# Kernel tuning notes

Measured on AMD Instinct MI355X. Metric: run time of the kernel, lower is better.

Reference implementation:

```python
import jax, jax.numpy as jnp
import numpy as np

NEG_SLOPE = 0.2  # PyG GATConv default negative_slope


def _gat_conv(x, edge_index, W, a_src, a_dst, b, concat):
    """One PyG-style GATConv layer (eval mode, add_self_loops=True).
    x: [N, F_in], W: [F_in, H*C], a_src/a_dst: [H, C], b: [H*C] or [C].
    """
    N = x.shape[0]
    H, C = a_src.shape
    loops = jnp.arange(N, dtype=edge_index.dtype)
    src = jnp.concatenate([edge_index[0], loops])  # [E+N]
    dst = jnp.concatenate([edge_index[1], loops])
    h = (x @ W).reshape(N, H, C)                   # [N,H,C]
    al_s = jnp.einsum('nhc,hc->nh', h, a_src)      # [N,H]
    al_d = jnp.einsum('nhc,hc->nh', h, a_dst)
    e = jax.nn.leaky_relu(al_s[src] + al_d[dst], NEG_SLOPE)  # [E+N, H]
    # segment softmax over incoming edges of each dst node
    m = jax.lax.stop_gradient(jax.ops.segment_max(e, dst, num_segments=N))
    ex = jnp.exp(e - m[dst])
    denom = jax.ops.segment_sum(ex, dst, num_segments=N)
    alpha = ex / denom[dst]                        # [E+N, H]
    out = jax.ops.segment_sum(h[src] * alpha[:, :, None], dst, num_segments=N)  # [N,H,C]
    out = out.reshape(N, H * C) if concat else out.mean(axis=1)
    return out + b


def setup_inputs() -> dict:
    key = jax.random.key(0)
    ks = jax.random.split(key, 10)
    N, E, F_IN = 100000, 1600000, 128
    H1, C1 = 4, 32   # layer 1: concat -> 128
    H2, C2 = 1, 64   # layer 2: mean   -> 64
    x = jax.random.normal(ks[0], (N, F_IN), dtype=jnp.float32)
    edge_index = jax.random.randint(ks[1], (2, E), 0, N, dtype=jnp.int32)
    s = 0.1
    return {
        'x': x,
        'edge_index': edge_index,
        'W1': jax.random.normal(ks[2], (F_IN, H1 * C1), dtype=jnp.float32) * s,
        'a1_src': jax.random.normal(ks[3], (H1, C1), dtype=jnp.float32) * s,
        'a1_dst': jax.random.normal(ks[4], (H1, C1), dtype=jnp.float32) * s,
        'b1': jnp.zeros((H1 * C1,), dtype=jnp.float32),
        'W2': jax.random.normal(ks[5], (H1 * C1, H2 * C2), dtype=jnp.float32) * s,
        'a2_src': jax.random.normal(ks[6], (H2, C2), dtype=jnp.float32) * s,
        'a2_dst': jax.random.normal(ks[7], (H2, C2), dtype=jnp.float32) * s,
        'b2': jnp.zeros((C2,), dtype=jnp.float32),
    }


def reference(x, edge_index, W1, a1_src, a1_dst, b1, W2, a2_src, a2_dst, b2):
    h = _gat_conv(x, edge_index, W1, a1_src, a1_dst, b1, concat=True)   # [N,128]
    h = jax.nn.elu(h)                                                   # dropout is identity in eval
    out = _gat_conv(h, edge_index, W2, a2_src, a2_dst, b2, concat=False)  # [N,64]
    return out
```

## Files before the change

kernel.cpp:

```cpp
#include <hip/hip_runtime.h>
#include <hip/hip_bf16.h>
#include <math.h>

static constexpr float NEG_SLOPE = 0.2f;
static constexpr float NEG_BIG = -3.0e38f;

typedef __attribute__((ext_vector_type(8))) short short8;
typedef __attribute__((ext_vector_type(4))) float f32x4;

__device__ __forceinline__ float blo(unsigned u) { return __uint_as_float(u << 16); }
__device__ __forceinline__ float bhi(unsigned u) { return __uint_as_float(u & 0xffff0000u); }
__device__ __forceinline__ float bhiraw(unsigned u) { return __uint_as_float(u); }
__device__ __forceinline__ unsigned pack2(float a, float b) {
  __hip_bfloat162 t = __float22bfloat162_rn(make_float2(a, b));
  union { __hip_bfloat162 b; unsigned u; } v;
  v.b = t;
  return v.u;
}

#define FMA8(V, A)                         \
  acc[0] = fmaf(blo((V).x), (A), acc[0]);  \
  acc[1] = fmaf(bhi((V).x), (A), acc[1]);  \
  acc[2] = fmaf(blo((V).y), (A), acc[2]);  \
  acc[3] = fmaf(bhi((V).y), (A), acc[3]);  \
  acc[4] = fmaf(blo((V).z), (A), acc[4]);  \
  acc[5] = fmaf(bhi((V).z), (A), acc[5]);  \
  acc[6] = fmaf(blo((V).w), (A), acc[6]);  \
  acc[7] = fmaf(bhi((V).w), (A), acc[7])

#define FMA8R(V, A)                           \
  acc[0] = fmaf(blo((V).x), (A), acc[0]);     \
  acc[1] = fmaf(bhiraw((V).x), (A), acc[1]);  \
  acc[2] = fmaf(blo((V).y), (A), acc[2]);     \
  acc[3] = fmaf(bhiraw((V).y), (A), acc[3]);  \
  acc[4] = fmaf(blo((V).z), (A), acc[4]);     \
  acc[5] = fmaf(bhiraw((V).z), (A), acc[5]);  \
  acc[6] = fmaf(blo((V).w), (A), acc[6]);     \
  acc[7] = fmaf(bhiraw((V).w), (A), acc[7])

template <int BN, int HEADS>
__device__ void prep_w(const float* __restrict__ W, const float* __restrict__ as_,
                       const float* __restrict__ ad_, uint4* __restrict__ out, int i) {
  constexpr int XC = BN + 16;
  constexpr int C = BN / HEADS;
  if (i >= XC * 16) return;
  const int col = i >> 4;
  const int chunk = (i & 15) ^ (col & 7);
  float v[8];
  if (col < BN) {
#pragma unroll
    for (int t = 0; t < 8; ++t) v[t] = W[(size_t)(chunk * 8 + t) * BN + col];
  } else {
    const int j = col - BN;
#pragma unroll
    for (int t = 0; t < 8; ++t) v[t] = 0.f;
    if (j < 2 * HEADS) {
      const int hh = (HEADS == 4) ? (j & 3) : 0;
      const bool is_src = (HEADS == 4) ? (j < 4) : (j == 0);
      const float* av = (is_src ? as_ : ad_) + hh * C;
      const float* wb = W + hh * C;
#pragma unroll
      for (int t = 0; t < 8; ++t) {
        float s = 0.f;
        for (int c = 0; c < C; ++c) s = fmaf(wb[(size_t)(chunk * 8 + t) * BN + c], av[c], s);
        v[t] = s;
      }
    }
  }
  uint4 u;
  u.x = pack2(v[0], v[1]);
  u.y = pack2(v[2], v[3]);
  u.z = pack2(v[4], v[5]);
  u.w = pack2(v[6], v[7]);
  out[i] = u;
}

__global__ void k_setup(const float* __restrict__ W1, const float* __restrict__ a1s,
                        const float* __restrict__ a1d, uint4* __restrict__ wsw1,
                        const float* __restrict__ W2, const float* __restrict__ a2s,
                        const float* __restrict__ a2d, uint4* __restrict__ wsw2,
                        int* __restrict__ cnt, int N) {
  const int b = blockIdx.x;
  const int tid = threadIdx.x;
  if (b < 9) {
    prep_w<128, 4>(W1, a1s, a1d, wsw1, b * 256 + tid);
  } else if (b < 14) {
    prep_w<64, 1>(W2, a2s, a2d, wsw2, (b - 9) * 256 + tid);
  } else {
    const int i = (b - 14) * 256 + tid;
    if (i < (N >> 2)) ((int4*)cnt)[i] = make_int4(0, 0, 0, 0);
    const int r = (N & ~3) + i;
    if (i < 4 && r < N) cnt[r] = 0;
  }
}

template <int BN, int HEADS>
__global__ __launch_bounds__(256) void k_mfma_gemm(
    const float* __restrict__ x, const uint4* __restrict__ wsw,
    __hip_bfloat16* __restrict__ h_out, float* __restrict__ als,
    float* __restrict__ ald, int N) {
  constexpr int XC = BN + 16;
  constexpr int NTILES = BN / 16;
  constexpr int BUFSZ = (XC * 256 > 128 * 256) ? XC * 256 : 128 * 256;
  __shared__ unsigned char buf[BUFSZ];
  const int tid = threadIdx.x;
  const int lane = tid & 63;
  const int wid = tid >> 6;
  const int base = blockIdx.x * 128;

  for (int it = 0; it < 8; ++it) {
    const int i = it * 256 + tid;
    const int r = i >> 4, c = i & 15;
    const int g = base + r;
    float4 f0 = make_float4(0.f, 0.f, 0.f, 0.f), f1 = f0;
    if (g < N) {
      const float* xp = x + (size_t)g * 128 + c * 8;
      f0 = *(const float4*)xp;
      f1 = *(const float4*)(xp + 4);
    }
    uint4 u;
    u.x = pack2(f0.x, f0.y);
    u.y = pack2(f0.z, f0.w);
    u.z = pack2(f1.x, f1.y);
    u.w = pack2(f1.z, f1.w);
    *(uint4*)(buf + r * 256 + ((c * 16) ^ ((r & 7) << 4))) = u;
  }
  __syncthreads();

  const int lg = lane >> 4;
  const int ll = lane & 15;
  union U { uint4 u; short8 s; };
  short8 afr[2][4];
#pragma unroll
  for (int rt = 0; rt < 2; ++rt) {
    const int row = wid * 32 + rt * 16 + ll;
    const unsigned char* rp = buf + row * 256;
    const int swz = (row & 7) << 4;
#pragma unroll
    for (int ks = 0; ks < 4; ++ks) {
      U t;
      t.u = *(const uint4*)(rp + ((ks * 64 + lg * 16) ^ swz));
      afr[rt][ks] = t.s;
    }
  }
  __syncthreads();

  {
    uint4* dst = (uint4*)buf;
    for (int i = tid; i < XC * 16; i += 256) dst[i] = wsw[i];
  }
  __syncthreads();

  f32x4 acc[2][NTILES + 1];
#pragma unroll
  for (int rt = 0; rt < 2; ++rt)
#pragma unroll
    for (int t = 0; t <= NTILES; ++t) acc[rt][t] = (f32x4){0.f, 0.f, 0.f, 0.f};

#pragma unroll
  for (int t = 0; t <= NTILES; ++t) {
    const int col = t * 16 + ll;
    const unsigned char* cp = buf + col * 256;
    const int swz = (col & 7) << 4;
#pragma unroll
    for (int ks = 0; ks < 4; ++ks) {
      U b;
      b.u = *(const uint4*)(cp + ((ks * 64 + lg * 16) ^ swz));
      acc[0][t] = __builtin_amdgcn_mfma_f32_16x16x32_bf16(afr[0][ks], b.s, acc[0][t], 0, 0, 0);
      acc[1][t] = __builtin_amdgcn_mfma_f32_16x16x32_bf16(afr[1][ks], b.s, acc[1][t], 0, 0, 0);
    }
  }

#pragma unroll
  for (int rt = 0; rt < 2; ++rt) {
#pragma unroll
    for (int r = 0; r < 4; ++r) {
      const int row = base + wid * 32 + rt * 16 + lg * 4 + r;
      if (row < N) {
        const float v = acc[rt][NTILES][r];
        if (HEADS == 4) {
          if (ll < 4) als[(size_t)row * 4 + ll] = v;
          else if (ll < 8) ald[(size_t)row * 4 + (ll - 4)] = v;
        } else {
          if (ll == 0) als[row] = v;
          else if (ll == 1) ald[row] = v;
        }
      }
    }
  }

  __syncthreads();
#pragma unroll
  for (int rt = 0; rt < 2; ++rt) {
#pragma unroll
    for (int t = 0; t < NTILES; ++t) {
#pragma unroll
      for (int r = 0; r < 4; ++r) {
        const float v = acc[rt][t][r];
        const float vn = __shfl_xor(v, 1, 64);
        if (!(lane & 1)) {
          const int row = wid * 32 + rt * 16 + lg * 4 + r;
          *(unsigned*)(buf + row * (BN * 2) + (t * 16 + ll) * 2) = pack2(v, vn);
        }
      }
    }
  }
  __syncthreads();
  {
    constexpr int U4 = 128 * BN / 8;
    constexpr int U4R = BN / 8;
    for (int i = tid; i < U4; i += 256) {
      const int row = i / U4R;
      const int g = base + row;
      if (g < N)
        *(uint4*)((unsigned short*)h_out + (size_t)g * BN + (i % U4R) * 8) = ((uint4*)buf)[i];
    }
  }
}

__global__ void k_count(const int* __restrict__ edst, int* __restrict__ cnt, int E) {
  int i = blockIdx.x * blockDim.x + threadIdx.x;
  if (i < E) atomicAdd(cnt + edst[i], 1);
}

__global__ void k_scan_local(const int* __restrict__ cnt, int* __restrict__ rowptr,
                             int* __restrict__ bsum, int N) {
  __shared__ int lds[256];
  const int tid = threadIdx.x;
  const int base = blockIdx.x * 1024;
  int vals[4], tsum = 0;
#pragma unroll
  for (int q = 0; q < 4; ++q) {
    int i = base + tid * 4 + q;
    vals[q] = (i < N) ? cnt[i] + 1 : 0;
    tsum += vals[q];
  }
  lds[tid] = tsum;
  __syncthreads();
  for (int off = 1; off < 256; off <<= 1) {
    int t = (tid >= off) ? lds[tid - off] : 0;
    __syncthreads();
    lds[tid] += t;
    __syncthreads();
  }
  int run = lds[tid] - tsum;
  if (tid == 255) bsum[blockIdx.x] = lds[255];
#pragma unroll
  for (int q = 0; q < 4; ++q) {
    int i = base + tid * 4 + q;
    if (i < N) rowptr[i] = run;
    run += vals[q];
  }
}

__global__ void k_scan_add2(const int* __restrict__ bsum, int nb,
                            int* __restrict__ rowptr, int* __restrict__ cursor,
                            int N, int total) {
  __shared__ int pref[128];
  const int tid = threadIdx.x;
  int own = 0;
  if (tid < 128) {
    own = (tid < nb) ? bsum[tid] : 0;
    pref[tid] = own;
  }
  __syncthreads();
  for (int off = 1; off < 128; off <<= 1) {
    int t = (tid >= off && tid < 128) ? pref[tid - off] : 0;
    __syncthreads();
    if (tid < 128) pref[tid] += t;
    __syncthreads();
  }
  if (tid < 128) pref[tid] -= own;
  __syncthreads();
  const int i = blockIdx.x * blockDim.x + tid;
  if (i < N) {
    int r = rowptr[i] + pref[i >> 10];
    rowptr[i] = r;
    cursor[i] = r;
  } else if (i == N) {
    rowptr[N] = total;
  }
}

__global__ void k_build_part(const int* __restrict__ esrc, const int* __restrict__ edst,
                             int* __restrict__ cursor, int* __restrict__ nbr, int E, int N) {
  constexpr int NPARTS = 4;
  const int p = blockIdx.x & 3;
  const int span = (N + NPARTS - 1) / NPARTS;
  const int lo = p * span;
  const int hi = min(N, lo + span);
  const int gid = (int)(blockIdx.x >> 2) * blockDim.x + threadIdx.x;
  const int stride = (int)(gridDim.x >> 2) * blockDim.x;
  const int E4 = E >> 2;
  for (int i = gid; i < E4; i += stride) {
    const int4 d4 = ((const int4*)edst)[i];
    const int4 s4 = ((const int4*)esrc)[i];
    if (d4.x >= lo && d4.x < hi) nbr[atomicAdd(cursor + d4.x, 1)] = s4.x;
    if (d4.y >= lo && d4.y < hi) nbr[atomicAdd(cursor + d4.y, 1)] = s4.y;
    if (d4.z >= lo && d4.z < hi) nbr[atomicAdd(cursor + d4.z, 1)] = s4.z;
    if (d4.w >= lo && d4.w < hi) nbr[atomicAdd(cursor + d4.w, 1)] = s4.w;
  }
  for (int i = E4 * 4 + gid; i < E + N; i += stride) {
    const int d = i < E ? edst[i] : i - E;
    if (d >= lo && d < hi) {
      const int sn = i < E ? esrc[i] : i - E;
      nbr[atomicAdd(cursor + d, 1)] = sn;
    }
  }
}

__global__ void k_gather_l1(const int* __restrict__ rowptr, const int* __restrict__ nbr,
                            const float* __restrict__ als, const float* __restrict__ ald,
                            const __hip_bfloat16* __restrict__ hfeat,
                            const float* __restrict__ bias,
                            float* __restrict__ out, int N) {
  __shared__ float atab[4][2][4][40];
  __shared__ unsigned otab[4][2][32];
  const int lane = threadIdx.x & 63;
  const int wid = threadIdx.x >> 6;
  const int half = lane >> 5;
  const int l32 = lane & 31;
  const int node = (int)((blockIdx.x * blockDim.x + threadIdx.x) >> 6) * 2 + half;
  const bool valid = node < N;
  int start = 0, end = 0;
  if (valid) {
    start = rowptr[node];
    end = rowptr[node + 1];
  }
  const int deg = end - start;
  const float4 aldd = valid ? ((const float4*)ald)[node] : make_float4(0.f, 0.f, 0.f, 0.f);

  float t[4];
  int myn = 0;
  {
    const int j = start + l32;
    if (j < end) {
      myn = nbr[j];
      const float4 av = ((const float4*)als)[myn];
      const float tr[4] = {av.x + aldd.x, av.y + aldd.y, av.z + aldd.z, av.w + aldd.w};
#pragma unroll
      for (int h = 0; h < 4; ++h) t[h] = tr[h] >= 0.f ? tr[h] : NEG_SLOPE * tr[h];
    } else {
#pragma unroll
      for (int h = 0; h < 4; ++h) t[h] = NEG_BIG;
    }
  }
  otab[wid][half][l32] = (unsigned)myn << 8;

  float Mh[4], rden[4], myex[4];
  if (deg <= 32) {
#pragma unroll
    for (int h = 0; h < 4; ++h) {
      float M = t[h];
#pragma unroll
      for (int off = 1; off < 32; off <<= 1) M = fmaxf(M, __shfl_xor(M, off, 64));
      const float e = __expf(t[h] - M);
      float sum = e;
#pragma unroll
      for (int off = 1; off < 32; off <<= 1) sum += __shfl_xor(sum, off, 64);
      Mh[h] = M;
      rden[h] = 1.f / sum;
      myex[h] = e * rden[h];
    }
  } else {
    float m[4], s[4];
#pragma unroll
    for (int h = 0; h < 4; ++h) {
      m[h] = t[h];
      s[h] = (t[h] > NEG_BIG) ? 1.f : 0.f;
    }
    for (int b = start + 32; b < end; b += 32) {
      const int j = b + l32;
      if (j < end) {
        const int sn = nbr[j];
        const float4 av = ((const float4*)als)[sn];
        const float tr[4] = {av.x + aldd.x, av.y + aldd.y, av.z + aldd.z, av.w + aldd.w};
#pragma unroll
        for (int h = 0; h < 4; ++h) {
          const float tv = tr[h] >= 0.f ? tr[h] : NEG_SLOPE * tr[h];
          const float M = fmaxf(m[h], tv);
          s[h] = s[h] * __expf(m[h] - M) + __expf(tv - M);
          m[h] = M;
        }
      }
    }
#pragma unroll
    for (int h = 0; h < 4; ++h) {
      float M = m[h];
#pragma unroll
      for (int off = 1; off < 32; off <<= 1) M = fmaxf(M, __shfl_xor(M, off, 64));
      float e = s[h] * __expf(m[h] - M);
#pragma unroll
      for (int off = 1; off < 32; off <<= 1) e += __shfl_xor(e, off, 64);
      Mh[h] = M;
      rden[h] = 1.f / e;
      myex[h] = __expf(t[h] - M) * rden[h];
    }
  }
#pragma unroll
  for (int h = 0; h < 4; ++h) atab[wid][half][h][l32] = myex[h];

  const int sub = l32 >> 4;
  const int q = l32 & 15;
  const int head = q >> 2;
  const char* hq = (const char*)hfeat + q * 16;
  float acc[8];
#pragma unroll
  for (int k = 0; k < 8; ++k) acc[k] = 0.f;

  const int nq = deg < 32 ? deg : 32;
  const float* ap = &atab[wid][half][head][0];
  const unsigned* op = &otab[wid][half][0];
  for (int j0 = 0; j0 < nq; j0 += 8) {
    const float a0 = ap[j0 + sub];
    const float a1 = ap[j0 + 2 + sub];
    const float a2 = ap[j0 + 4 + sub];
    const float a3 = ap[j0 + 6 + sub];
    const uint4 v0 = *(const uint4*)(hq + op[j0 + sub]);
    const uint4 v1 = *(const uint4*)(hq + op[j0 + 2 + sub]);
    const uint4 v2 = *(const uint4*)(hq + op[j0 + 4 + sub]);
    const uint4 v3 = *(const uint4*)(hq + op[j0 + 6 + sub]);
    FMA8R(v0, a0);
    FMA8R(v1, a1);
    FMA8R(v2, a2);
    FMA8R(v3, a3);
  }
  if (deg > 32) {
    const float Mm = head == 0 ? Mh[0] : head == 1 ? Mh[1] : head == 2 ? Mh[2] : Mh[3];
    const float rd = head == 0 ? rden[0] : head == 1 ? rden[1] : head == 2 ? rden[2] : rden[3];
    const float ad_ = head == 0 ? aldd.x : head == 1 ? aldd.y : head == 2 ? aldd.z : aldd.w;
    for (int j0 = 32; j0 < deg; j0 += 2) {
      const int j = j0 + sub;
      float a = 0.f;
      int sn = 0;
      if (j < deg) {
        sn = nbr[start + j];
        const float4 av = ((const float4*)als)[sn];
        const float as_ = head == 0 ? av.x : head == 1 ? av.y : head == 2 ? av.z : av.w;
        float tv = as_ + ad_;
        tv = tv >= 0.f ? tv : NEG_SLOPE * tv;
        a = __expf(tv - Mm) * rd;
      }
      const uint4 v = *(const uint4*)(hq + (size_t)sn * 256);
      FMA8R(v, a);
    }
  }

#pragma unroll
  for (int k = 0; k < 8; ++k) acc[k] += __shfl_xor(acc[k], 16, 64);
  if (valid && sub == 0) {
    const float4 b0 = ((const float4*)bias)[q * 2];
    const float4 b1 = ((const float4*)bias)[q * 2 + 1];
    float r[8] = {acc[0] + b0.x, acc[1] + b0.y, acc[2] + b0.z, acc[3] + b0.w,
                  acc[4] + b1.x, acc[5] + b1.y, acc[6] + b1.z, acc[7] + b1.w};
#pragma unroll
    for (int k = 0; k < 8; ++k) r[k] = r[k] > 0.f ? r[k] : __expf(r[k]) - 1.f;
    float4* opo = (float4*)(out + (size_t)node * 128 + q * 8);
    opo[0] = make_float4(r[0], r[1], r[2], r[3]);
    opo[1] = make_float4(r[4], r[5], r[6], r[7]);
  }
}

__global__ void k_gather_l2(const int* __restrict__ rowptr, const int* __restrict__ nbr,
                            const float* __restrict__ als, const float* __restrict__ ald,
                            const __hip_bfloat16* __restrict__ hfeat,
                            const float* __restrict__ bias,
                            float* __restrict__ out, int N) {
  __shared__ float2 atab[4][2][36];
  const int lane = threadIdx.x & 63;
  const int wid = threadIdx.x >> 6;
  const int half = lane >> 5;
  const int l32 = lane & 31;
  const int node = (int)((blockIdx.x * blockDim.x + threadIdx.x) >> 6) * 2 + half;
  const bool valid = node < N;
  int start = 0, end = 0;
  if (valid) {
    start = rowptr[node];
    end = rowptr[node + 1];
  }
  const int deg = end - start;
  const float ald0 = valid ? ald[node] : 0.f;

  float t = NEG_BIG;
  int myn = 0;
  {
    const int j = start + l32;
    if (j < end) {
      myn = nbr[j];
      float tv = als[myn] + ald0;
      t = tv >= 0.f ? tv : NEG_SLOPE * tv;
    }
  }

  float M, rden, myal;
  if (deg <= 32) {
    M = t;
#pragma unroll
    for (int off = 1; off < 32; off <<= 1) M = fmaxf(M, __shfl_xor(M, off, 64));
    const float e = __expf(t - M);
    float sum = e;
#pragma unroll
    for (int off = 1; off < 32; off <<= 1) sum += __shfl_xor(sum, off, 64);
    rden = 1.f / sum;
    myal = e * rden;
  } else {
    float m = t, s = (t > NEG_BIG) ? 1.f : 0.f;
    for (int b = start + 32; b < end; b += 32) {
      const int j = b + l32;
      if (j < end) {
        float tv = als[nbr[j]] + ald0;
        tv = tv >= 0.f ? tv : NEG_SLOPE * tv;
        const float Mn = fmaxf(m, tv);
        s = s * __expf(m - Mn) + __expf(tv - Mn);
        m = Mn;
      }
    }
    M = m;
#pragma unroll
    for (int off = 1; off < 32; off <<= 1) M = fmaxf(M, __shfl_xor(M, off, 64));
    float e = s * __expf(m - M);
#pragma unroll
    for (int off = 1; off < 32; off <<= 1) e += __shfl_xor(e, off, 64);
    rden = 1.f / e;
    myal = __expf(t - M) * rden;
  }
  atab[wid][half][l32] = make_float2(myal, __int_as_float(myn << 7));

  const int sub = l32 >> 3;
  const int q = l32 & 7;
  const char* hq = (const char*)hfeat + q * 16;
  float acc[8];
#pragma unroll
  for (int k = 0; k < 8; ++k) acc[k] = 0.f;

  const int nq = deg < 32 ? deg : 32;
  const float2* ap = &atab[wid][half][0];
  for (int j0 = 0; j0 < nq; j0 += 16) {
    const float2 o0 = ap[j0 + sub];
    const float2 o1 = ap[j0 + 4 + sub];
    const float2 o2 = ap[j0 + 8 + sub];
    const float2 o3 = ap[j0 + 12 + sub];
    const uint4 v0 = *(const uint4*)(hq + (unsigned)__float_as_int(o0.y));
    const uint4 v1 = *(const uint4*)(hq + (unsigned)__float_as_int(o1.y));
    const uint4 v2 = *(const uint4*)(hq + (unsigned)__float_as_int(o2.y));
    const uint4 v3 = *(const uint4*)(hq + (unsigned)__float_as_int(o3.y));
    FMA8(v0, o0.x);
    FMA8(v1, o1.x);
    FMA8(v2, o2.x);
    FMA8(v3, o3.x);
  }
  if (deg > 32) {
    for (int j0 = 32; j0 < deg; j0 += 4) {
      const int j = j0 + sub;
      float a = 0.f;
      int sn = 0;
      if (j < deg) {
        sn = nbr[start + j];
        float tv = als[sn] + ald0;
        tv = tv >= 0.f ? tv : NEG_SLOPE * tv;
        a = __expf(tv - M) * rden;
      }
      const uint4 v = *(const uint4*)(hq + (size_t)sn * 128);
      FMA8(v, a);
    }
  }

#pragma unroll
  for (int k = 0; k < 8; ++k) {
    acc[k] += __shfl_xor(acc[k], 8, 64);
    acc[k] += __shfl_xor(acc[k], 16, 64);
  }
  if (valid && sub == 0) {
    const float4 b0 = ((const float4*)bias)[q * 2];
    const float4 b1 = ((const float4*)bias)[q * 2 + 1];
    float4* opo = (float4*)(out + (size_t)node * 64 + q * 8);
    opo[0] = make_float4(acc[0] + b0.x, acc[1] + b0.y, acc[2] + b0.z, acc[3] + b0.w);
    opo[1] = make_float4(acc[4] + b1.x, acc[5] + b1.y, acc[6] + b1.z, acc[7] + b1.w);
  }
}

extern "C" void kernel_launch(void* const* d_in, const int* in_sizes, int n_in,
                              void* d_out, int out_size, void* d_ws, size_t ws_size,
                              hipStream_t stream) {
  const float* x   = (const float*)d_in[0];
  const int*   ei  = (const int*)d_in[1];
  const float* W1  = (const float*)d_in[2];
  const float* a1s = (const float*)d_in[3];
  const float* a1d = (const float*)d_in[4];
  const float* b1  = (const float*)d_in[5];
  const float* W2  = (const float*)d_in[6];
  const float* a2s = (const float*)d_in[7];
  const float* a2d = (const float*)d_in[8];
  const float* b2  = (const float*)d_in[9];

  const int N = in_sizes[0] / 128;
  const int E = in_sizes[1] / 2;
  const int* esrc = ei;
  const int* edst = ei + E;

  float* ws   = (float*)d_ws;
  __hip_bfloat16* h = (__hip_bfloat16*)ws;
  float* out1 = ws   + (size_t)N * 128;
  float* als  = out1 + (size_t)N * 128;
  float* ald  = als  + (size_t)N * 4;
  int* cnt    = (int*)(ald + (size_t)N * 4);
  int* rowptr = cnt + N;
  int* cursor = rowptr + N + 1;
  int* bsum   = cursor + N;
  int* nbr    = bsum + 1024;
  size_t off = ((size_t)((nbr + E + N) - (int*)ws) + 3) & ~(size_t)3;
  uint4* wsw1 = (uint4*)((int*)ws + off);
  uint4* wsw2 = wsw1 + 144 * 16;

  float* outF = (float*)d_out;

  const int total = E + N;
  const int nb = (N + 1023) / 1024;

  const int zb = ((N >> 2) + 255) / 256;
  k_setup<<<14 + zb, 256, 0, stream>>>(W1, a1s, a1d, wsw1, W2, a2s, a2d, wsw2, cnt, N);
  k_count<<<(E + 255) / 256, 256, 0, stream>>>(edst, cnt, E);
  k_scan_local<<<nb, 256, 0, stream>>>(cnt, rowptr, bsum, N);
  k_scan_add2<<<(N + 256) / 256, 256, 0, stream>>>(bsum, nb, rowptr, cursor, N, total);
  k_build_part<<<1280, 256, 0, stream>>>(esrc, edst, cursor, nbr, E, N);

  k_mfma_gemm<128, 4><<<(N + 127) / 128, 256, 0, stream>>>(x, wsw1, h, als, ald, N);
  k_gather_l1<<<(N + 7) / 8, 256, 0, stream>>>(rowptr, nbr, als, ald, h, b1, out1, N);

  k_mfma_gemm<64, 1><<<(N + 127) / 128, 256, 0, stream>>>(out1, wsw2, h, als, ald, N);
  k_gather_l2<<<(N + 7) / 8, 256, 0, stream>>>(rowptr, nbr, als, ald, h, b2, outF, N);
}
```

Measured before the change: 320.4 us.

## Co-schedule CSR build and layer-1 GEMM in one launch; vectorize edge counting

Merges the CSR neighbor-list build and the layer-1 MFMA GEMM into a single kernel, split by block index, so the atomic-bound scatter and the compute-bound GEMM can share the GPU at the same time. The count kernel now has each thread handle four destinations through a vector load, and edge index reads use nontemporal loads. The risks are that the fused kernel takes the larger shared-memory footprint of the GEMM for every block, which can lower occupancy of the build blocks, and that block scheduling order decides how much actual overlap happens.

```diff
diff --git a/kernel.cpp b/kernel.cpp
--- a/kernel.cpp
+++ b/kernel.cpp
@@ -7,6 +7,7 @@
 
 typedef __attribute__((ext_vector_type(8))) short short8;
 typedef __attribute__((ext_vector_type(4))) float f32x4;
+typedef __attribute__((ext_vector_type(4))) int i32x4;
 
 __device__ __forceinline__ float blo(unsigned u) { return __uint_as_float(u << 16); }
 __device__ __forceinline__ float bhi(unsigned u) { return __uint_as_float(u & 0xffff0000u); }
@@ -16,6 +17,9 @@
   union { __hip_bfloat162 b; unsigned u; } v;
   v.b = t;
   return v.u;
+}
+__device__ __forceinline__ i32x4 ntload4(const int* p) {
+  return __builtin_nontemporal_load((const i32x4*)p);
 }
 
 #define FMA8(V, A)                         \
@@ -95,10 +99,9 @@
 }
 
 template <int BN, int HEADS>
-__global__ __launch_bounds__(256) void k_mfma_gemm(
-    const float* __restrict__ x, const uint4* __restrict__ wsw,
-    __hip_bfloat16* __restrict__ h_out, float* __restrict__ als,
-    float* __restrict__ ald, int N) {
+__device__ void gemm_body(const float* __restrict__ x, const uint4* __restrict__ wsw,
+                          __hip_bfloat16* __restrict__ h_out, float* __restrict__ als,
+                          float* __restrict__ ald, int N, int bid) {
   constexpr int XC = BN + 16;
   constexpr int NTILES = BN / 16;
   constexpr int BUFSZ = (XC * 256 > 128 * 256) ? XC * 256 : 128 * 256;
@@ -106,7 +109,7 @@
   const int tid = threadIdx.x;
   const int lane = tid & 63;
   const int wid = tid >> 6;
-  const int base = blockIdx.x * 128;
+  const int base = bid * 128;
 
   for (int it = 0; it < 8; ++it) {
     const int i = it * 256 + tid;
@@ -218,9 +221,69 @@
   }
 }
 
+template <int BN, int HEADS>
+__global__ __launch_bounds__(256) void k_mfma_gemm(
+    const float* __restrict__ x, const uint4* __restrict__ wsw,
+    __hip_bfloat16* __restrict__ h_out, float* __restrict__ als,
+    float* __restrict__ ald, int N) {
+  gemm_body<BN, HEADS>(x, wsw, h_out, als, ald, N, blockIdx.x);
+}
+
+__device__ void build_body(const int* __restrict__ esrc, const int* __restrict__ edst,
+                           int* __restrict__ cursor, int* __restrict__ nbr, int E, int N,
+                           int bid, int nbuild) {
+  constexpr int NPARTS = 4;
+  const int p = bid & 3;
+  const int span = (N + NPARTS - 1) / NPARTS;
+  const int lo = p * span;
+  const int hi = min(N, lo + span);
+  const int gid = (bid >> 2) * 256 + (int)threadIdx.x;
+  const int stride = (nbuild >> 2) * 256;
+  const int E4 = E >> 2;
+  for (int i = gid; i < E4; i += stride) {
+    const i32x4 d4 = ntload4(edst + i * 4);
+    const i32x4 s4 = ntload4(esrc + i * 4);
+    if (d4.x >= lo && d4.x < hi) nbr[atomicAdd(cursor + d4.x, 1)] = s4.x;
+    if (d4.y >= lo && d4.y < hi) nbr[atomicAdd(cursor + d4.y, 1)] = s4.y;
+    if (d4.z >= lo && d4.z < hi) nbr[atomicAdd(cursor + d4.z, 1)] = s4.z;
+    if (d4.w >= lo && d4.w < hi) nbr[atomicAdd(cursor + d4.w, 1)] = s4.w;
+  }
+  for (int i = E4 * 4 + gid; i < E + N; i += stride) {
+    const int d = i < E ? edst[i] : i - E;
+    if (d >= lo && d < hi) {
+      const int sn = i < E ? esrc[i] : i - E;
+      nbr[atomicAdd(cursor + d, 1)] = sn;
+    }
+  }
+}
+
+__global__ __launch_bounds__(256) void k_build_gemm1(
+    const int* __restrict__ esrc, const int* __restrict__ edst,
+    int* __restrict__ cursor, int* __restrict__ nbr, int E, int nbuild,
+    const float* __restrict__ x, const uint4* __restrict__ wsw,
+    __hip_bfloat16* __restrict__ h_out, float* __restrict__ als,
+    float* __restrict__ ald, int N) {
+  const int b = (int)blockIdx.x;
+  if (b < nbuild) {
+    build_body(esrc, edst, cursor, nbr, E, N, b, nbuild);
+    return;
+  }
+  gemm_body<128, 4>(x, wsw, h_out, als, ald, N, b - nbuild);
+}
+
 __global__ void k_count(const int* __restrict__ edst, int* __restrict__ cnt, int E) {
   int i = blockIdx.x * blockDim.x + threadIdx.x;
-  if (i < E) atomicAdd(cnt + edst[i], 1);
+  const int E4 = E >> 2;
+  if (i < E4) {
+    const i32x4 d4 = ntload4(edst + i * 4);
+    atomicAdd(cnt + d4.x, 1);
+    atomicAdd(cnt + d4.y, 1);
+    atomicAdd(cnt + d4.z, 1);
+    atomicAdd(cnt + d4.w, 1);
+  } else {
+    const int r = E4 * 4 + (i - E4);
+    if (r < E) atomicAdd(cnt + edst[r], 1);
+  }
 }
 
 __global__ void k_scan_local(const int* __restrict__ cnt, int* __restrict__ rowptr,
@@ -279,33 +342,6 @@
     cursor[i] = r;
   } else if (i == N) {
     rowptr[N] = total;
-  }
-}
-
-__global__ void k_build_part(const int* __restrict__ esrc, const int* __restrict__ edst,
-                             int* __restrict__ cursor, int* __restrict__ nbr, int E, int N) {
-  constexpr int NPARTS = 4;
-  const int p = blockIdx.x & 3;
-  const int span = (N + NPARTS - 1) / NPARTS;
-  const int lo = p * span;
-  const int hi = min(N, lo + span);
-  const int gid = (int)(blockIdx.x >> 2) * blockDim.x + threadIdx.x;
-  const int stride = (int)(gridDim.x >> 2) * blockDim.x;
-  const int E4 = E >> 2;
-  for (int i = gid; i < E4; i += stride) {
-    const int4 d4 = ((const int4*)edst)[i];
-    const int4 s4 = ((const int4*)esrc)[i];
-    if (d4.x >= lo && d4.x < hi) nbr[atomicAdd(cursor + d4.x, 1)] = s4.x;
-    if (d4.y >= lo && d4.y < hi) nbr[atomicAdd(cursor + d4.y, 1)] = s4.y;
-    if (d4.z >= lo && d4.z < hi) nbr[atomicAdd(cursor + d4.z, 1)] = s4.z;
-    if (d4.w >= lo && d4.w < hi) nbr[atomicAdd(cursor + d4.w, 1)] = s4.w;
-  }
-  for (int i = E4 * 4 + gid; i < E + N; i += stride) {
-    const int d = i < E ? edst[i] : i - E;
-    if (d >= lo && d < hi) {
-      const int sn = i < E ? esrc[i] : i - E;
-      nbr[atomicAdd(cursor + d, 1)] = sn;
-    }
   }
 }
 
@@ -616,15 +652,18 @@
 
   const int total = E + N;
   const int nb = (N + 1023) / 1024;
+  const int nbuild = 1280;
+  const int ngemm1 = (N + 127) / 128;
 
   const int zb = ((N >> 2) + 255) / 256;
   k_setup<<<14 + zb, 256, 0, stream>>>(W1, a1s, a1d, wsw1, W2, a2s, a2d, wsw2, cnt, N);
-  k_count<<<(E + 255) / 256, 256, 0, stream>>>(edst, cnt, E);
+  k_count<<<((E >> 2) + (E & 3) + 255) / 256, 256, 0, stream>>>(edst, cnt, E);
   k_scan_local<<<nb, 256, 0, stream>>>(cnt, rowptr, bsum, N);
   k_scan_add2<<<(N + 256) / 256, 256, 0, stream>>>(bsum, nb, rowptr, cursor, N, total);
-  k_build_part<<<1280, 256, 0, stream>>>(esrc, edst, cursor, nbr, E, N);
-
-  k_mfma_gemm<128, 4><<<(N + 127) / 128, 256, 0, stream>>>(x, wsw1, h, als, ald, N);
+
+  k_build_gemm1<<<nbuild + ngemm1, 256, 0, stream>>>(
+      esrc, edst, cursor, nbr, E, nbuild, x, wsw1, h, als, ald, N);
+
   k_gather_l1<<<(N + 7) / 8, 256, 0, stream>>>(rowptr, nbr, als, ald, h, b1, out1, N);
 
   k_mfma_gemm<64, 1><<<(N + 127) / 128, 256, 0, stream>>>(out1, wsw2, h, als, ald, N);
```

Result: faster. 300.4 us (-6.3%).
